# Performance work log

Hardware: AMD Instinct MI355X
Metric: run time of the kernel (lower is better)

## Reference

```python
import jax, jax.numpy as jnp
import numpy as np

VOCAB, E, H, L, B, T = 32000, 64, 8, 25, 1000, 512


def setup_inputs() -> dict:
    key = jax.random.key(0)
    ks = jax.random.split(key, 6)
    return {
        "x": jax.random.randint(ks[0], (B, T), 0, VOCAB),
        "h_0": jnp.zeros((L, B, H), jnp.float32),
        "embedding": jax.random.normal(ks[1], (VOCAB, E), jnp.float32) * 0.02,
        "W_xh0": jax.random.normal(ks[2], (E, H), jnp.float32) / np.float32(np.sqrt(E)),
        "W_xh_rest": jax.random.normal(ks[3], (L - 1, H, H), jnp.float32) / np.float32(np.sqrt(H)),
        "W_hh": jax.random.normal(ks[4], (L, H, H), jnp.float32) / np.float32(np.sqrt(H)),
        "b_h": jnp.zeros((L, H), jnp.float32),
        "W_hy": jax.random.normal(ks[5], (H, 1), jnp.float32) / np.float32(np.sqrt(H)),
        "b_y": jnp.zeros((1,), jnp.float32),
    }


def reference(x, h_0, embedding, W_xh0, W_xh_rest, W_hh, b_h, W_hy, b_y):
    # x: [B, T] int ids; embedded: [B, T, E]
    emb = embedding[x]
    n_layers = h_0.shape[0]

    def step(h, e_t):  # h: [L, B, H], e_t: [B, E]
        inp = e_t
        hs = []
        for i in range(n_layers):  # fixed small layer count -> unrolled
            W = W_xh0 if i == 0 else W_xh_rest[i - 1]
            h_i = jnp.tanh(inp @ W + h[i] @ W_hh[i] + b_h[i])
            hs.append(h_i)
            inp = h_i
        return jnp.stack(hs, 0), None

    h_last, _ = jax.lax.scan(step, h_0, jnp.swapaxes(emb, 0, 1))  # scan over time
    logits = h_last[-1] @ W_hy + b_y  # [B, 1]
    return logits.squeeze(1), h_last
```

## Files before the change

### kernel.cpp

```cpp
#include <hip/hip_runtime.h>

#define VOCAB 32000
#define E 64
#define H 8
#define L 25
#define B 1000
#define T 512

#define CHUNK 8
#define NCHUNK (T / CHUNK)
#define NSTEP (NCHUNK + L - 1)
#define THREADS 256

#define LAYER_STRIDE 132
#define LDS_FLOATS ((L + 1) * LAYER_STRIDE)

#define SCALE 2.8853900817779268f

typedef float v2f __attribute__((ext_vector_type(2)));
typedef float v4f __attribute__((ext_vector_type(4)));

__device__ __forceinline__ v2f pk_fma(v2f a, v2f b, v2f c) {
    v2f d;
    asm("v_pk_fma_f32 %0, %1, %2, %3" : "=v"(d) : "v"(a), "v"(b), "v"(c));
    return d;
}
__device__ __forceinline__ v2f pk_mul(v2f a, v2f b) {
    v2f d;
    asm("v_pk_mul_f32 %0, %1, %2" : "=v"(d) : "v"(a), "v"(b));
    return d;
}
__device__ __forceinline__ v2f pk_add(v2f a, v2f b) {
    v2f d;
    asm("v_pk_add_f32 %0, %1, %2" : "=v"(d) : "v"(a), "v"(b));
    return d;
}

__global__ __launch_bounds__(256) void proj_kernel(
    const float* __restrict__ emb, const float* __restrict__ w0,
    const float* __restrict__ bh, float* __restrict__ ptab)
{
    __shared__ float w0s[E * H];
    int tid = threadIdx.x;
    w0s[tid] = w0[tid];
    w0s[tid + 256] = w0[tid + 256];
    __syncthreads();

    int r = blockIdx.x * 256 + tid;
    if (r >= VOCAB) return;
    const float4* e4 = (const float4*)(emb + r * E);
    const v2f* w2 = (const v2f*)w0s;
    v2f a0 = {0.f, 0.f}, a1 = {0.f, 0.f}, a2 = {0.f, 0.f}, a3 = {0.f, 0.f};
#pragma unroll
    for (int k4 = 0; k4 < E / 4; ++k4) {
        float4 v = e4[k4];
        int kb = k4 * 16;
        a0 = pk_fma((v2f){v.x, v.x}, w2[kb + 0], a0);
        a1 = pk_fma((v2f){v.x, v.x}, w2[kb + 1], a1);
        a2 = pk_fma((v2f){v.x, v.x}, w2[kb + 2], a2);
        a3 = pk_fma((v2f){v.x, v.x}, w2[kb + 3], a3);
        a0 = pk_fma((v2f){v.y, v.y}, w2[kb + 4], a0);
        a1 = pk_fma((v2f){v.y, v.y}, w2[kb + 5], a1);
        a2 = pk_fma((v2f){v.y, v.y}, w2[kb + 6], a2);
        a3 = pk_fma((v2f){v.y, v.y}, w2[kb + 7], a3);
        a0 = pk_fma((v2f){v.z, v.z}, w2[kb + 8], a0);
        a1 = pk_fma((v2f){v.z, v.z}, w2[kb + 9], a1);
        a2 = pk_fma((v2f){v.z, v.z}, w2[kb + 10], a2);
        a3 = pk_fma((v2f){v.z, v.z}, w2[kb + 11], a3);
        a0 = pk_fma((v2f){v.w, v.w}, w2[kb + 12], a0);
        a1 = pk_fma((v2f){v.w, v.w}, w2[kb + 13], a1);
        a2 = pk_fma((v2f){v.w, v.w}, w2[kb + 14], a2);
        a3 = pk_fma((v2f){v.w, v.w}, w2[kb + 15], a3);
    }
    float4 b0 = *(const float4*)bh;
    float4 b1 = *(const float4*)(bh + 4);
    float4* o4 = (float4*)(ptab + r * 8);
    o4[0] = (float4){(a0.x + b0.x) * SCALE, (a0.y + b0.y) * SCALE,
                     (a1.x + b0.z) * SCALE, (a1.y + b0.w) * SCALE};
    o4[1] = (float4){(a2.x + b1.x) * SCALE, (a2.y + b1.y) * SCALE,
                     (a3.x + b1.z) * SCALE, (a3.y + b1.w) * SCALE};
}

__device__ __forceinline__ float qp1(float x) {
    return __int_as_float(__builtin_amdgcn_mov_dpp(__float_as_int(x), 0xB1, 0xF, 0xF, true));
}
__device__ __forceinline__ float qp2(float x) {
    return __int_as_float(__builtin_amdgcn_mov_dpp(__float_as_int(x), 0x4E, 0xF, 0xF, true));
}
__device__ __forceinline__ float ror8(float x) {
    return __int_as_float(__builtin_amdgcn_mov_dpp(__float_as_int(x), 0x128, 0xF, 0xF, true));
}

__global__ __launch_bounds__(THREADS) void rnn_recur(
    const int*   __restrict__ x,
    const float* __restrict__ h0,
    const float* __restrict__ wrest,
    const float* __restrict__ whh_g,
    const float* __restrict__ bh,
    const float* __restrict__ why,
    const float* __restrict__ by,
    const float* __restrict__ ptab,
    float*       __restrict__ out)
{
    __shared__ __align__(16) float buf[LDS_FLOATS];

    const int tid = threadIdx.x;
    for (int k = tid; k < LDS_FLOATS; k += THREADS) buf[k] = 0.f;

    const int row = tid >> 4;
    const int lp  = tid & 15;
    const int j   = (lp & 3) | ((lp >> 3) << 2);
    const int g   = row * 2 + ((lp >> 2) & 1);
    const bool active = g < L;
    const int gc  = active ? g : 0;
    const int b = blockIdx.x;

    v2f wh01 = {0.f, 0.f}, wh23 = {0.f, 0.f}, wh45 = {0.f, 0.f}, wh67 = {0.f, 0.f};
    v2f wx01 = {0.f, 0.f}, wx23 = {0.f, 0.f}, wx45 = {0.f, 0.f}, wx67 = {0.f, 0.f};
    v2f h01  = {0.f, 0.f}, h23  = {0.f, 0.f}, h45  = {0.f, 0.f}, h67  = {0.f, 0.f};
    float pv[CHUNK];

    float* mybuf = &buf[gc * LAYER_STRIDE];
    const float* prevbuf = (gc > 0) ? (mybuf - LAYER_STRIDE)
                                    : (&buf[L * LAYER_STRIDE]);

    if (active) {
        const float* whL = whh_g + g * 64;
        wh01 = (v2f){whL[(j ^ 0) * 8 + j], whL[(j ^ 1) * 8 + j]} * SCALE;
        wh23 = (v2f){whL[(j ^ 2) * 8 + j], whL[(j ^ 3) * 8 + j]} * SCALE;
        wh45 = (v2f){whL[(j ^ 4) * 8 + j], whL[(j ^ 5) * 8 + j]} * SCALE;
        wh67 = (v2f){whL[(j ^ 6) * 8 + j], whL[(j ^ 7) * 8 + j]} * SCALE;
        if (g > 0) {
            const float* wxL = wrest + (g - 1) * 64;
            wx01 = (v2f){wxL[0 * 8 + j], wxL[1 * 8 + j]} * SCALE;
            wx23 = (v2f){wxL[2 * 8 + j], wxL[3 * 8 + j]} * SCALE;
            wx45 = (v2f){wxL[4 * 8 + j], wxL[5 * 8 + j]} * SCALE;
            wx67 = (v2f){wxL[6 * 8 + j], wxL[7 * 8 + j]} * SCALE;
        }
        const float* h0p = h0 + (g * B + b) * H;
        h01 = (v2f){h0p[j ^ 0], h0p[j ^ 1]};
        h23 = (v2f){h0p[j ^ 2], h0p[j ^ 3]};
        h45 = (v2f){h0p[j ^ 4], h0p[j ^ 5]};
        h67 = (v2f){h0p[j ^ 6], h0p[j ^ 7]};
        float bs = bh[g * 8 + j] * SCALE;
#pragma unroll
        for (int ct = 0; ct < CHUNK; ++ct) pv[ct] = bs;
    }

    const int xbase = b * T;
    if (active && g == 0) {
#pragma unroll
        for (int ct = 0; ct < CHUNK; ++ct)
            pv[ct] = ptab[x[xbase + ct] * H + j];
    }
    __syncthreads();

    for (int s = 0; s < NSTEP; ++s) {
        const int c = s - g;
        if (active && (unsigned)c < (unsigned)NCHUNK) {
            const int p = c & 1;
            float* wptr = mybuf + p * (CHUNK * 8);
            const v4f* ip4 = (const v4f*)(prevbuf + p * (CHUNK * 8));

            int4 t0, t1;
            const bool pf = (g == 0) && (c + 1 < NCHUNK);
            if (pf) {
                const int4* xp4 = (const int4*)(x + xbase + (c + 1) * CHUNK);
                t0 = xp4[0];
                t1 = xp4[1];
            }

            v4f ia = ip4[0], ib = ip4[1];
#pragma unroll
            for (int ct = 0; ct < CHUNK; ++ct) {
                v4f ian = ia, ibn = ib;
                if (ct < CHUNK - 1) {
                    ian = ip4[2 * ct + 2];
                    ibn = ip4[2 * ct + 3];
                }
                v2f i01 = __builtin_shufflevector(ia, ia, 0, 1);
                v2f i23 = __builtin_shufflevector(ia, ia, 2, 3);
                v2f i45 = __builtin_shufflevector(ib, ib, 0, 1);
                v2f i67 = __builtin_shufflevector(ib, ib, 2, 3);

                v2f acc0 = pk_mul(i01, wx01);
                v2f acc1 = pk_mul(i23, wx23);
                acc0 = pk_fma(i45, wx45, acc0);
                acc1 = pk_fma(i67, wx67, acc1);
                acc0 = pk_fma(h01, wh01, acc0);
                acc1 = pk_fma(h23, wh23, acc1);
                acc0 = pk_fma(h45, wh45, acc0);
                acc1 = pk_fma(h67, wh67, acc1);
                acc0 = pk_add(acc0, acc1);
                float arg = acc0.x + acc0.y + pv[ct];
                float tt = __builtin_amdgcn_exp2f(arg);
                float rc = __builtin_amdgcn_rcpf(1.0f + tt);
                float hn = __builtin_fmaf(-2.0f, rc, 1.0f);

                wptr[ct * 8 + j] = hn;

                float o1 = qp1(hn);
                float q0 = qp2(hn);
                float q1 = qp2(o1);
                h01 = (v2f){hn, o1};
                h23 = (v2f){q0, q1};
                h45 = (v2f){ror8(hn), ror8(o1)};
                h67 = (v2f){ror8(q0), ror8(q1)};

                ia = ian;
                ib = ibn;
            }

            if (pf) {
                pv[0] = ptab[t0.x * H + j];
                pv[1] = ptab[t0.y * H + j];
                pv[2] = ptab[t0.z * H + j];
                pv[3] = ptab[t0.w * H + j];
                pv[4] = ptab[t1.x * H + j];
                pv[5] = ptab[t1.y * H + j];
                pv[6] = ptab[t1.z * H + j];
                pv[7] = ptab[t1.w * H + j];
            }

            if (c == NCHUNK - 1) {
                out[B + (g * B + b) * H + j] = h01.x;
                if (g == L - 1) {
                    float v = h01.x * why[j];
                    v += qp1(v);
                    v += qp2(v);
                    v += ror8(v);
                    if (j == 0) out[b] = v + by[0];
                }
            }
        }
        __syncthreads();
    }
}

extern "C" void kernel_launch(void* const* d_in, const int* in_sizes, int n_in,
                              void* d_out, int out_size, void* d_ws, size_t ws_size,
                              hipStream_t stream) {
    const int*   x     = (const int*)d_in[0];
    const float* h0    = (const float*)d_in[1];
    const float* emb   = (const float*)d_in[2];
    const float* w0    = (const float*)d_in[3];
    const float* wrest = (const float*)d_in[4];
    const float* whh   = (const float*)d_in[5];
    const float* bh    = (const float*)d_in[6];
    const float* why   = (const float*)d_in[7];
    const float* by    = (const float*)d_in[8];
    float* out  = (float*)d_out;
    float* ptab = (float*)d_ws;

    hipLaunchKernelGGL(proj_kernel, dim3((VOCAB + 255) / 256), dim3(256),
                       0, stream, emb, w0, bh, ptab);
    hipLaunchKernelGGL(rnn_recur, dim3(B), dim3(THREADS),
                       0, stream, x, h0, wrest, whh, bh, why, by, ptab, out);
}
```

Measured before the change: 222.7 us.

## Restructure embedding projection to stage rows in LDS with one thread per output

The vocabulary projection kernel now loads 32 embedding rows per block into padded shared memory with coalesced float4 loads, and has each thread compute a single output element. This replaces the one-row-per-thread scheme whose strided per-thread global reads were poorly coalesced and which launched only 125 blocks. The grid grows to 1000 blocks for more parallelism, at the cost of LDS staging and redundant reads of the weights from shared memory. The recurrent kernel, which likely dominates total time, is unchanged.

```diff
diff --git a/kernel.cpp b/kernel.cpp
--- a/kernel.cpp
+++ b/kernel.cpp
@@ -36,49 +36,45 @@
     return d;
 }
 
+#define PROJ_ROWS 32
+#define ESTRIDE 65
 __global__ __launch_bounds__(256) void proj_kernel(
     const float* __restrict__ emb, const float* __restrict__ w0,
     const float* __restrict__ bh, float* __restrict__ ptab)
 {
+    __shared__ float es[PROJ_ROWS * ESTRIDE];
     __shared__ float w0s[E * H];
-    int tid = threadIdx.x;
+
+    const int tid = threadIdx.x;
     w0s[tid] = w0[tid];
     w0s[tid + 256] = w0[tid + 256];
+
+    const float4* e4 = (const float4*)(emb) + (size_t)blockIdx.x * (PROJ_ROWS * E / 4);
+#pragma unroll
+    for (int it = 0; it < 2; ++it) {
+        int idx = tid + it * 256;
+        float4 v = e4[idx];
+        int r  = idx >> 4;
+        int k0 = (idx & 15) * 4;
+        float* d = &es[r * ESTRIDE + k0];
+        d[0] = v.x; d[1] = v.y; d[2] = v.z; d[3] = v.w;
+    }
     __syncthreads();
 
-    int r = blockIdx.x * 256 + tid;
-    if (r >= VOCAB) return;
-    const float4* e4 = (const float4*)(emb + r * E);
-    const v2f* w2 = (const v2f*)w0s;
-    v2f a0 = {0.f, 0.f}, a1 = {0.f, 0.f}, a2 = {0.f, 0.f}, a3 = {0.f, 0.f};
-#pragma unroll
-    for (int k4 = 0; k4 < E / 4; ++k4) {
-        float4 v = e4[k4];
-        int kb = k4 * 16;
-        a0 = pk_fma((v2f){v.x, v.x}, w2[kb + 0], a0);
-        a1 = pk_fma((v2f){v.x, v.x}, w2[kb + 1], a1);
-        a2 = pk_fma((v2f){v.x, v.x}, w2[kb + 2], a2);
-        a3 = pk_fma((v2f){v.x, v.x}, w2[kb + 3], a3);
-        a0 = pk_fma((v2f){v.y, v.y}, w2[kb + 4], a0);
-        a1 = pk_fma((v2f){v.y, v.y}, w2[kb + 5], a1);
-        a2 = pk_fma((v2f){v.y, v.y}, w2[kb + 6], a2);
-        a3 = pk_fma((v2f){v.y, v.y}, w2[kb + 7], a3);
-        a0 = pk_fma((v2f){v.z, v.z}, w2[kb + 8], a0);
-        a1 = pk_fma((v2f){v.z, v.z}, w2[kb + 9], a1);
-        a2 = pk_fma((v2f){v.z, v.z}, w2[kb + 10], a2);
-        a3 = pk_fma((v2f){v.z, v.z}, w2[kb + 11], a3);
-        a0 = pk_fma((v2f){v.w, v.w}, w2[kb + 12], a0);
-        a1 = pk_fma((v2f){v.w, v.w}, w2[kb + 13], a1);
-        a2 = pk_fma((v2f){v.w, v.w}, w2[kb + 14], a2);
-        a3 = pk_fma((v2f){v.w, v.w}, w2[kb + 15], a3);
-    }
-    float4 b0 = *(const float4*)bh;
-    float4 b1 = *(const float4*)(bh + 4);
-    float4* o4 = (float4*)(ptab + r * 8);
-    o4[0] = (float4){(a0.x + b0.x) * SCALE, (a0.y + b0.y) * SCALE,
-                     (a1.x + b0.z) * SCALE, (a1.y + b0.w) * SCALE};
-    o4[1] = (float4){(a2.x + b1.x) * SCALE, (a2.y + b1.y) * SCALE,
-                     (a3.x + b1.z) * SCALE, (a3.y + b1.w) * SCALE};
+    const int r = tid >> 3;
+    const int j = tid & 7;
+    const float* e = &es[r * ESTRIDE];
+    float a0 = 0.f, a1 = 0.f, a2 = 0.f, a3 = 0.f;
+#pragma unroll
+    for (int k = 0; k < E; k += 4) {
+        a0 = __builtin_fmaf(e[k + 0], w0s[(k + 0) * H + j], a0);
+        a1 = __builtin_fmaf(e[k + 1], w0s[(k + 1) * H + j], a1);
+        a2 = __builtin_fmaf(e[k + 2], w0s[(k + 2) * H + j], a2);
+        a3 = __builtin_fmaf(e[k + 3], w0s[(k + 3) * H + j], a3);
+    }
+    float dot = (a0 + a1) + (a2 + a3);
+    int row = blockIdx.x * PROJ_ROWS + r;
+    ptab[row * H + j] = (dot + bh[j]) * SCALE;
 }
 
 __device__ __forceinline__ float qp1(float x) {
@@ -252,7 +248,7 @@
     float* out  = (float*)d_out;
     float* ptab = (float*)d_ws;
 
-    hipLaunchKernelGGL(proj_kernel, dim3((VOCAB + 255) / 256), dim3(256),
+    hipLaunchKernelGGL(proj_kernel, dim3(VOCAB / PROJ_ROWS), dim3(256),
                        0, stream, emb, w0, bh, ptab);
     hipLaunchKernelGGL(rnn_recur, dim3(B), dim3(THREADS),
                        0, stream, x, h0, wrest, whh, bh, why, by, ptab, out);
```

After: 222.5 us. About the same (-0.1%).
